# Performance work log

Hardware: AMD Instinct MI355X
Metric: run time of the kernel (lower is better)

The kernel has to match this reference:

```python
import jax, jax.numpy as jnp
import numpy as np

# FreeConv2D: locally-connected 2D conv (unshared per-location kernels) + bias.
# out[b,oh,ow,u] = sum_{i,j,c} w[oh,ow,u,i,j,c] * x[b, oh*s1+i, ow*s2+j, c] + bias[oh,ow,u]

B, H, W, C = 64, 64, 64, 64
U, K, S = 64, 5, 2
OH = (H - K) // S + 1  # 30 (== ceil((H-K+1)/S))
OW = (W - K) // S + 1  # 30


def setup_inputs() -> dict:
    key = jax.random.key(0)
    kx, kw, kb = jax.random.split(key, 3)
    x = jax.random.normal(kx, (B, H, W, C), dtype=jnp.float32)
    w = jax.random.normal(kw, (OH, OW, U, K, K, C), dtype=jnp.float32) * 0.05
    b = jax.random.normal(kb, (OH, OW, U), dtype=jnp.float32) * 0.05
    return {"x": x, "w": w, "b": b}


def reference(x, w, b):
    s1 = s2 = S
    # Accumulate over the small fixed kernel window (K*K = 25 taps);
    # each tap is a per-location contraction over channels (batched GEMV).
    out = jnp.zeros((x.shape[0], OH, OW, U), dtype=x.dtype)
    for i in range(K):
        for j in range(K):
            # x_slice[b,oh,ow,c] = x[b, oh*s1+i, ow*s2+j, c]
            x_slice = x[:, i:i + (OH - 1) * s1 + 1:s1, j:j + (OW - 1) * s2 + 1:s2, :]
            out = out + jnp.einsum('bhwc,hwuc->bhwu', x_slice, w[:, :, :, i, j, :])
    return out + b  # activation is None (identity)
```

## Files before the change

### kernel.cpp

```cpp
#include <hip/hip_runtime.h>


typedef __bf16 bf16x8 __attribute__((ext_vector_type(8)));
typedef float f32x4 __attribute__((ext_vector_type(4)));

__device__ __forceinline__ unsigned short f2bf(float f) {
    unsigned int u = __float_as_uint(f);
    u += 0x7FFFu + ((u >> 16) & 1u);
    return (unsigned short)(u >> 16);
}


__global__ __launch_bounds__(256, 4)
void freeconv_kernel(const float* __restrict__ x,
                     const float* __restrict__ w,
                     const float* __restrict__ bias,
                     float* __restrict__ out) {
    __shared__ __align__(16) unsigned short ldsA[10240];
    __shared__ __align__(16) unsigned short ldsB[10240];

    const int bid = blockIdx.x;
    const int oh = bid / 30;
    const int ow = bid - oh * 30;
    const int t = threadIdx.x;
    const int lane = t & 63;
    const int wave = t >> 6;
    const int wm = wave >> 1;
    const int wn = wave & 1;

    const int swz = ((lane >> 4) << 7) + (((lane & 15) ^ (lane >> 4)) << 3);

    int rr[10], cc[10], ww[10];
#pragma unroll
    for (int it = 0; it < 10; ++it) {
        int g = it * 256 + t;
        int r = g / 40;
        int k = (g - r * 40) * 4;
        rr[it] = r;
        cc[it] = k;
        int grp = (k >> 3) & 3;
        ww[it] = ((k >> 5) * 4 + (r >> 4)) * 512 + grp * 128 + (((r & 15) ^ grp) * 8) + (k & 7);
    }

    f32x4 acc[2][2];
#pragma unroll
    for (int a = 0; a < 2; ++a)
#pragma unroll
        for (int b2 = 0; b2 < 2; ++b2)
#pragma unroll
            for (int r = 0; r < 4; ++r) acc[a][b2][r] = 0.f;

    const float* wblk = w + (oh * 30 + ow) * 102400;

    for (int ci = 0; ci < 10; ++ci) {
        const int i  = ci >> 1;
        const int kh = ci & 1;
        const int aoff = (oh * 2 + i) * 4096 + ow * 128 + kh * 160;
        const int boff = i * 320 + kh * 160;

#pragma unroll
        for (int bt = 0; bt < 2; ++bt) {
            float4 va[5], vb[5];
#pragma unroll
            for (int q = 0; q < 5; ++q) {
                int it = bt * 5 + q;
                va[q] = *(const float4*)(x + rr[it] * 262144 + aoff + cc[it]);
            }
#pragma unroll
            for (int q = 0; q < 5; ++q) {
                int it = bt * 5 + q;
                vb[q] = *(const float4*)(wblk + rr[it] * 1600 + boff + cc[it]);
            }
#pragma unroll
            for (int q = 0; q < 5; ++q) {
                int it = bt * 5 + q;
                ushort4 pv;
                pv.x = f2bf(va[q].x); pv.y = f2bf(va[q].y);
                pv.z = f2bf(va[q].z); pv.w = f2bf(va[q].w);
                *(ushort4*)&ldsA[ww[it]] = pv;
            }
#pragma unroll
            for (int q = 0; q < 5; ++q) {
                int it = bt * 5 + q;
                ushort4 pv;
                pv.x = f2bf(vb[q].x); pv.y = f2bf(vb[q].y);
                pv.z = f2bf(vb[q].z); pv.w = f2bf(vb[q].w);
                *(ushort4*)&ldsB[ww[it]] = pv;
            }
        }
        __syncthreads();

#pragma unroll
        for (int ks = 0; ks < 5; ++ks) {
            const bf16x8 a0 = *(const bf16x8*)&ldsA[(ks * 4 + wm * 2 + 0) * 512 + swz];
            const bf16x8 a1 = *(const bf16x8*)&ldsA[(ks * 4 + wm * 2 + 1) * 512 + swz];
            const bf16x8 b0 = *(const bf16x8*)&ldsB[(ks * 4 + wn * 2 + 0) * 512 + swz];
            const bf16x8 b1 = *(const bf16x8*)&ldsB[(ks * 4 + wn * 2 + 1) * 512 + swz];
            acc[0][0] = __builtin_amdgcn_mfma_f32_16x16x32_bf16(a0, b0, acc[0][0], 0, 0, 0);
            acc[0][1] = __builtin_amdgcn_mfma_f32_16x16x32_bf16(a0, b1, acc[0][1], 0, 0, 0);
            acc[1][0] = __builtin_amdgcn_mfma_f32_16x16x32_bf16(a1, b0, acc[1][0], 0, 0, 0);
            acc[1][1] = __builtin_amdgcn_mfma_f32_16x16x32_bf16(a1, b1, acc[1][1], 0, 0, 0);
        }
        __syncthreads();
    }

    const float* bp = bias + (oh * 30 + ow) * 64;
    const int col = lane & 15;
    const int r0 = (lane >> 4) * 4;
    float bv0 = bp[wn * 32 + col];
    float bv1 = bp[wn * 32 + 16 + col];
#pragma unroll
    for (int ms = 0; ms < 2; ++ms) {
#pragma unroll
        for (int r = 0; r < 4; ++r) {
            int bi = wm * 32 + ms * 16 + r0 + r;
            float* op = out + ((bi * 30 + oh) * 30 + ow) * 64 + wn * 32 + col;
            op[0]  = acc[ms][0][r] + bv0;
            op[16] = acc[ms][1][r] + bv1;
        }
    }
}

extern "C" void kernel_launch(void* const* d_in, const int* in_sizes, int n_in,
                              void* d_out, int out_size, void* d_ws, size_t ws_size,
                              hipStream_t stream) {
    const float* x = (const float*)d_in[0];
    const float* w = (const float*)d_in[1];
    const float* b = (const float*)d_in[2];
    float* out = (float*)d_out;
    (void)in_sizes; (void)n_in; (void)out_size; (void)d_ws; (void)ws_size;
    freeconv_kernel<<<dim3(900), dim3(256), 0, stream>>>(x, w, b, out);
}
```

Before: 563.9 us.

## Stage fp32 tiles into LDS via direct global-to-LDS DMA, convert to bf16 at fragment load

The register-staged load/convert/store path is replaced by global_load_lds DMA that copies raw fp32 tiles straight into LDS. The fp32-to-bf16 conversion moves to fragment-read time using a round-to-nearest-even add plus a byte permute. The K loop is re-tiled from 10 chunks of 160 to 25 chunks of 64 channels, one per tap. This aims to cut VGPR traffic and the LDS write instructions. In exchange it doubles the LDS footprint per element, adds more barriers per block, and repeats the conversion for each wave that reads a fragment.

```diff
diff --git a/kernel.cpp b/kernel.cpp
--- a/kernel.cpp
+++ b/kernel.cpp
@@ -1,114 +1,114 @@
 #include <hip/hip_runtime.h>
+#include <stdint.h>
 
 
 typedef __bf16 bf16x8 __attribute__((ext_vector_type(8)));
 typedef float f32x4 __attribute__((ext_vector_type(4)));
 
-__device__ __forceinline__ unsigned short f2bf(float f) {
-    unsigned int u = __float_as_uint(f);
-    u += 0x7FFFu + ((u >> 16) & 1u);
-    return (unsigned short)(u >> 16);
+typedef __attribute__((address_space(1))) uint32_t glob_u32;
+typedef __attribute__((address_space(3))) uint32_t lds_u32;
+
+__device__ __forceinline__ void dma16(const void* g, void* l) {
+    __builtin_amdgcn_global_load_lds(
+        (const glob_u32*)(uintptr_t)g,
+        (lds_u32*)(uint32_t)(uintptr_t)l,
+        16, 0, 0);
+}
+
+__device__ __forceinline__ unsigned brne(unsigned a) {
+    return a + 0x7FFFu + ((a >> 16) & 1u);
 }
 
 
-__global__ __launch_bounds__(256, 4)
+__device__ __forceinline__ bf16x8 cvt_frag(const float* p) {
+    const uint4 a = *(const uint4*)p;
+    const uint4 b = *(const uint4*)(p + 256);
+    union { unsigned u[4]; bf16x8 v; } r;
+    r.u[0] = __builtin_amdgcn_perm(brne(a.y), brne(a.x), 0x07060302);
+    r.u[1] = __builtin_amdgcn_perm(brne(a.w), brne(a.z), 0x07060302);
+    r.u[2] = __builtin_amdgcn_perm(brne(b.y), brne(b.x), 0x07060302);
+    r.u[3] = __builtin_amdgcn_perm(brne(b.w), brne(b.z), 0x07060302);
+    return r.v;
+}
+
+__global__ __launch_bounds__(256)
 void freeconv_kernel(const float* __restrict__ x,
                      const float* __restrict__ w,
                      const float* __restrict__ bias,
                      float* __restrict__ out) {
-    __shared__ __align__(16) unsigned short ldsA[10240];
-    __shared__ __align__(16) unsigned short ldsB[10240];
+    __shared__ __align__(16) float ldsA[4096];
+    __shared__ __align__(16) float ldsB[4096];
 
     const int bid = blockIdx.x;
     const int oh = bid / 30;
     const int ow = bid - oh * 30;
     const int t = threadIdx.x;
     const int lane = t & 63;
-    const int wave = t >> 6;
-    const int wm = wave >> 1;
-    const int wn = wave & 1;
+    const int wv = t >> 6;
+    const int wvu = __builtin_amdgcn_readfirstlane(wv);
+    const int wm = wv >> 1;
+    const int wn = wv & 1;
 
-    const int swz = ((lane >> 4) << 7) + (((lane & 15) ^ (lane >> 4)) << 3);
-
-    int rr[10], cc[10], ww[10];
+    int ia[4], ib[4];
 #pragma unroll
-    for (int it = 0; it < 10; ++it) {
-        int g = it * 256 + t;
-        int r = g / 40;
-        int k = (g - r * 40) * 4;
-        rr[it] = r;
-        cc[it] = k;
-        int grp = (k >> 3) & 3;
-        ww[it] = ((k >> 5) * 4 + (r >> 4)) * 512 + grp * 128 + (((r & 15) ^ grp) * 8) + (k & 7);
+    for (int s = 0; s < 4; ++s) {
+        int fi = wv * 1024 + s * 256 + lane * 4;
+        int blk = fi >> 9;
+        int half = (fi >> 8) & 1;
+        int grp = (fi >> 6) & 3;
+        int mi = (fi >> 2) & 15;
+        int m = (blk & 3) * 16 + mi;
+        int kk = (blk >> 2) * 32 + grp * 8 + half * 4;
+        ia[s] = m * 262144 + kk;
+        ib[s] = m * 1600 + kk;
     }
 
     f32x4 acc[2][2];
 #pragma unroll
     for (int a = 0; a < 2; ++a)
 #pragma unroll
-        for (int b2 = 0; b2 < 2; ++b2)
+        for (int b = 0; b < 2; ++b)
 #pragma unroll
-            for (int r = 0; r < 4; ++r) acc[a][b2][r] = 0.f;
+            for (int r = 0; r < 4; ++r) acc[a][b][r] = 0.f;
 
     const float* wblk = w + (oh * 30 + ow) * 102400;
+    float* lA = ldsA + wvu * 1024;
+    float* lB = ldsB + wvu * 1024;
 
-    for (int ci = 0; ci < 10; ++ci) {
-        const int i  = ci >> 1;
-        const int kh = ci & 1;
-        const int aoff = (oh * 2 + i) * 4096 + ow * 128 + kh * 160;
-        const int boff = i * 320 + kh * 160;
+    for (int i = 0; i < 5; ++i) {
+        const float* pa_i = x + (oh * 2 + i) * 4096 + ow * 128;
+        const float* pb_i = wblk + i * 320;
+        for (int kh = 0; kh < 5; ++kh) {
+            const float* pa = pa_i + kh * 64;
+            const float* pb = pb_i + kh * 64;
+#pragma unroll
+            for (int s = 0; s < 4; ++s) {
+                dma16(pa + ia[s], lA + s * 256);
+                dma16(pb + ib[s], lB + s * 256);
+            }
+            __syncthreads();
 
 #pragma unroll
-        for (int bt = 0; bt < 2; ++bt) {
-            float4 va[5], vb[5];
-#pragma unroll
-            for (int q = 0; q < 5; ++q) {
-                int it = bt * 5 + q;
-                va[q] = *(const float4*)(x + rr[it] * 262144 + aoff + cc[it]);
+            for (int ks = 0; ks < 2; ++ks) {
+                const int rbase = (lane >> 4) * 64 + (lane & 15) * 4;
+                const bf16x8 a0 = cvt_frag(ldsA + (ks * 4 + wm * 2 + 0) * 512 + rbase);
+                const bf16x8 a1 = cvt_frag(ldsA + (ks * 4 + wm * 2 + 1) * 512 + rbase);
+                const bf16x8 b0 = cvt_frag(ldsB + (ks * 4 + wn * 2 + 0) * 512 + rbase);
+                const bf16x8 b1 = cvt_frag(ldsB + (ks * 4 + wn * 2 + 1) * 512 + rbase);
+                acc[0][0] = __builtin_amdgcn_mfma_f32_16x16x32_bf16(a0, b0, acc[0][0], 0, 0, 0);
+                acc[0][1] = __builtin_amdgcn_mfma_f32_16x16x32_bf16(a0, b1, acc[0][1], 0, 0, 0);
+                acc[1][0] = __builtin_amdgcn_mfma_f32_16x16x32_bf16(a1, b0, acc[1][0], 0, 0, 0);
+                acc[1][1] = __builtin_amdgcn_mfma_f32_16x16x32_bf16(a1, b1, acc[1][1], 0, 0, 0);
             }
-#pragma unroll
-            for (int q = 0; q < 5; ++q) {
-                int it = bt * 5 + q;
-                vb[q] = *(const float4*)(wblk + rr[it] * 1600 + boff + cc[it]);
-            }
-#pragma unroll
-            for (int q = 0; q < 5; ++q) {
-                int it = bt * 5 + q;
-                ushort4 pv;
-                pv.x = f2bf(va[q].x); pv.y = f2bf(va[q].y);
-                pv.z = f2bf(va[q].z); pv.w = f2bf(va[q].w);
-                *(ushort4*)&ldsA[ww[it]] = pv;
-            }
-#pragma unroll
-            for (int q = 0; q < 5; ++q) {
-                int it = bt * 5 + q;
-                ushort4 pv;
-                pv.x = f2bf(vb[q].x); pv.y = f2bf(vb[q].y);
-                pv.z = f2bf(vb[q].z); pv.w = f2bf(vb[q].w);
-                *(ushort4*)&ldsB[ww[it]] = pv;
-            }
+            __syncthreads();
         }
-        __syncthreads();
-
-#pragma unroll
-        for (int ks = 0; ks < 5; ++ks) {
-            const bf16x8 a0 = *(const bf16x8*)&ldsA[(ks * 4 + wm * 2 + 0) * 512 + swz];
-            const bf16x8 a1 = *(const bf16x8*)&ldsA[(ks * 4 + wm * 2 + 1) * 512 + swz];
-            const bf16x8 b0 = *(const bf16x8*)&ldsB[(ks * 4 + wn * 2 + 0) * 512 + swz];
-            const bf16x8 b1 = *(const bf16x8*)&ldsB[(ks * 4 + wn * 2 + 1) * 512 + swz];
-            acc[0][0] = __builtin_amdgcn_mfma_f32_16x16x32_bf16(a0, b0, acc[0][0], 0, 0, 0);
-            acc[0][1] = __builtin_amdgcn_mfma_f32_16x16x32_bf16(a0, b1, acc[0][1], 0, 0, 0);
-            acc[1][0] = __builtin_amdgcn_mfma_f32_16x16x32_bf16(a1, b0, acc[1][0], 0, 0, 0);
-            acc[1][1] = __builtin_amdgcn_mfma_f32_16x16x32_bf16(a1, b1, acc[1][1], 0, 0, 0);
-        }
-        __syncthreads();
     }
 
     const float* bp = bias + (oh * 30 + ow) * 64;
     const int col = lane & 15;
     const int r0 = (lane >> 4) * 4;
-    float bv0 = bp[wn * 32 + col];
-    float bv1 = bp[wn * 32 + 16 + col];
+    const float bv0 = bp[wn * 32 + col];
+    const float bv1 = bp[wn * 32 + 16 + col];
 #pragma unroll
     for (int ms = 0; ms < 2; ++ms) {
 #pragma unroll
```

Result: slower. 576.1 us (+2.2%).
